# Optimization experiments

Measured on AMD Instinct MI355X. Metric: run time of the kernel, lower is better.

The kernel has to match this reference:

```python
import jax, jax.numpy as jnp
import numpy as np

# (multiplicity, l) segments, ir_mul layout: each segment stored as (2l+1, mul)
IRREPS = [(256, 0), (256, 1), (256, 2), (256, 3)]
BATCH = 8192
DIM = sum(m * (2 * l + 1) for m, l in IRREPS)  # 4096


def _real_basis_U(l):
    """Unitary change of basis from complex to real spherical harmonics (degree l)."""
    n = 2 * l + 1
    U = np.zeros((n, n), dtype=np.complex128)
    U[l, l] = 1.0
    s = 1.0 / np.sqrt(2.0)
    for mu in range(1, l + 1):
        U[l + mu, l - mu] = s
        U[l + mu, l + mu] = s * (-1.0) ** mu
        U[l - mu, l - mu] = 1j * s
        U[l - mu, l + mu] = -1j * s * (-1.0) ** mu
    return U


def _x_generator_eig(l):
    """Eigendecomposition (constants) of the x-axis angular-momentum operator in the real basis."""
    m = np.arange(-l, l + 1)
    n = 2 * l + 1
    Jp = np.zeros((n, n), dtype=np.complex128)
    mm = m[:-1]
    Jp[np.arange(1, n), np.arange(0, n - 1)] = np.sqrt(l * (l + 1) - mm * (mm + 1))
    Jx = (Jp + Jp.conj().T) / 2.0
    U = _real_basis_U(l)
    Jx_r = U @ Jx @ U.conj().T  # Hermitian
    w, V = np.linalg.eigh(Jx_r)  # w = -l..l (integers), V unitary
    return w, V


def _y_rotation(theta, l):
    """Rotation about y in the real irrep basis, built directly from the angle
    encoding [cos(l t),...,cos(t),1,sin(t),...,sin(l t)] -- diag cos(m t), antidiag +/- sin(m t)."""
    B = theta.shape[0]
    n = 2 * l + 1
    mu = jnp.arange(1, l + 1, dtype=theta.dtype)
    c = jnp.cos(mu * theta[:, None])  # [B, l]
    s = jnp.sin(mu * theta[:, None])  # [B, l]
    one = jnp.ones((B, 1), theta.dtype)
    zero = jnp.zeros((B, 1), theta.dtype)
    diag = jnp.concatenate([c[:, ::-1], one, c], axis=-1)    # [B, n]
    anti = jnp.concatenate([-s[:, ::-1], zero, s], axis=-1)  # [B, n]
    idx = jnp.arange(n)
    R = jnp.zeros((B, n, n), theta.dtype)
    R = R.at[:, idx, idx].set(diag)
    R = R.at[:, idx, idx[::-1]].add(anti)
    return R


def _x_rotation(theta, l, dtype):
    """Rotation about x: X(t) = Re(V diag(exp(-i t w)) V^H), done in real arithmetic."""
    w, V = _x_generator_eig(l)
    w = jnp.asarray(w, dtype)
    Vr = jnp.asarray(np.ascontiguousarray(V.real), dtype)
    Vi = jnp.asarray(np.ascontiguousarray(V.imag), dtype)
    C = jnp.cos(theta[:, None] * w)  # [B, n]
    S = jnp.sin(theta[:, None] * w)  # [B, n]
    X = (jnp.einsum('ik,bk,jk->bij', Vr, C, Vr)
         + jnp.einsum('ik,bk,jk->bij', Vi, C, Vi)
         + jnp.einsum('ik,bk,jk->bij', Vi, S, Vr)
         - jnp.einsum('ik,bk,jk->bij', Vr, S, Vi))
    return X


def _rotate(gamma, beta, alpha, x):
    # yxy Euler rotation: first gamma about y, then beta about x, then alpha about y.
    outs = []
    off = 0
    for mul, l in IRREPS:
        n = 2 * l + 1
        seg = x[:, off:off + n * mul].reshape(-1, n, mul)  # ir_mul layout
        D = _y_rotation(alpha, l) @ _x_rotation(beta, l, x.dtype) @ _y_rotation(gamma, l)
        outs.append(jnp.einsum('bij,bjm->bim', D, seg).reshape(-1, n * mul))
        off += n * mul
    return jnp.concatenate(outs, axis=-1)


def setup_inputs() -> dict:
    key = jax.random.key(0)
    kg, kb, ka, kx = jax.random.split(key, 4)
    return {
        'gamma': jax.random.normal(kg, (BATCH,), jnp.float32),
        'beta': jax.random.normal(kb, (BATCH,), jnp.float32),
        'alpha': jax.random.normal(ka, (BATCH,), jnp.float32),
        'x': jax.random.normal(kx, (BATCH, DIM), jnp.float32),
    }


def reference(gamma, beta, alpha, x):
    return _rotate(gamma, beta, alpha, x)
```

## Files before the change

### kernel.cpp

```cpp
#include <hip/hip_runtime.h>
#include <math.h>

#define BATCH 8192
#define DIM 4096


struct FT { float v[495]; };

constexpr double csqrt(double x) {
  double g = x > 1.0 ? x : 1.0;
  for (int i = 0; i < 50; ++i) g = 0.5 * (g + x / g);
  return g;
}

constexpr void mmc(int n, const double* A, const double* B, double* C) {
  for (int i = 0; i < n; ++i)
    for (int j = 0; j < n; ++j) {
      double s = 0.0;
      for (int k = 0; k < n; ++k) s += A[i * n + k] * B[k * n + j];
      C[i * n + j] = s;
    }
}

constexpr FT compute_ft() {
  FT o{};
  for (int l = 1; l <= 3; ++l) {
    const int n = 2 * l + 1, nn = n * n;
    double JX[49] = {}, UR[49] = {}, UI[49] = {};
    for (int a = 0; a < n - 1; ++a) {
      double m = (double)(a - l);
      double v = 0.5 * csqrt((double)(l * (l + 1)) - m * (m + 1.0));
      JX[(a + 1) * n + a] = v;
      JX[a * n + (a + 1)] = v;
    }
    UR[l * n + l] = 1.0;
    const double s = csqrt(0.5);
    for (int mu = 1; mu <= l; ++mu) {
      double sg = (mu & 1) ? -1.0 : 1.0;
      UR[(l + mu) * n + (l - mu)] = s;
      UR[(l + mu) * n + (l + mu)] = s * sg;
      UI[(l - mu) * n + (l - mu)] = s;
      UI[(l - mu) * n + (l + mu)] = -s * sg;
    }
    double MR[49] = {}, MI[49] = {};
    mmc(n, UR, JX, MR);
    mmc(n, UI, JX, MI);
    double K[49] = {};
    for (int a = 0; a < n; ++a)
      for (int b = 0; b < n; ++b) {
        double acc = 0.0;
        for (int c = 0; c < n; ++c)
          acc += MI[a * n + c] * UR[b * n + c] - MR[a * n + c] * UI[b * n + c];
        K[a * n + b] = acc;
      }
    const double TH = 0.78539816339744830962;
    double S[49] = {}, P[49] = {}, T[49] = {};
    for (int i = 0; i < nn; ++i) S[i] = K[i] * (TH / 16.0);
    for (int i = 0; i < n; ++i) P[i * n + i] = 1.0;
    for (int t = 12; t >= 1; --t) {
      mmc(n, S, P, T);
      double inv = 1.0 / (double)t;
      for (int i = 0; i < nn; ++i) P[i] = T[i] * inv;
      for (int i = 0; i < n; ++i) P[i * n + i] += 1.0;
    }
    for (int q = 0; q < 4; ++q) {
      mmc(n, P, P, T);
      for (int i = 0; i < nn; ++i) P[i] = T[i];
    }
    double acc[7][49] = {};
    double Ek[49] = {}, Et[49] = {};
    for (int i = 0; i < n; ++i) Ek[i * n + i] = 1.0;
    const double r2 = csqrt(0.5);
    const double c8[8] = {1.0, r2, 0.0, -r2, -1.0, -r2, 0.0, r2};
    const double s8[8] = {0.0, r2, 1.0, r2, 0.0, -r2, -1.0, -r2};
    for (int k = 0; k < 8; ++k) {
      for (int i = 0; i < nn; ++i) acc[0][i] += 0.125 * Ek[i];
      for (int mu = 1; mu <= l; ++mu) {
        int a8 = (mu * k) & 7;
        double cc = 0.25 * c8[a8], ss = 0.25 * s8[a8];
        for (int i = 0; i < nn; ++i) {
          acc[2 * mu - 1][i] += cc * Ek[i];
          acc[2 * mu][i] += ss * Ek[i];
        }
      }
      mmc(n, Ek, P, Et);
      for (int i = 0; i < nn; ++i) Ek[i] = Et[i];
    }
    int base = (l == 1) ? 0 : ((l == 2) ? 27 : 152);
    for (int t = 0; t <= 2 * l; ++t)
      for (int i = 0; i < nn; ++i) o.v[base + t * nn + i] = (float)acc[t][i];
  }
  return o;
}

__device__ __constant__ FT c_tb = compute_ft();

typedef float vf4 __attribute__((ext_vector_type(4)));

__device__ __forceinline__ vf4 vfma4(float a, vf4 v, vf4 acc) { return acc + a * v; }

__device__ __forceinline__ float entry_for(int e, float cb1, float cb2, float cb3,
                                           float sb1, float sb2, float sb3,
                                           float al, float ga) {
  int l, n, basec, i, j;
  if (e < 9)       { l = 1; n = 3; basec = 0;   int r = e;      i = r / 3; j = r - i * 3; }
  else if (e < 34) { l = 2; n = 5; basec = 27;  int r = e - 9;  i = r / 5; j = r - i * 5; }
  else             { l = 3; n = 7; basec = 152; int r = e - 34; i = r / 7; j = r - i * 7; }

  const float* C = c_tb.v + basec;
  const int ip = n - 1 - i, jp = n - 1 - j;
  const int nn = n * n;
  float xij = 0.f, xijp = 0.f, xipj = 0.f, xipjp = 0.f;
  #pragma unroll
  for (int tt = 0; tt < 7; ++tt) {
    if (tt <= 2 * l) {
      float coef;
      if (tt == 0) coef = 1.f;
      else if (tt == 1) coef = cb1;
      else if (tt == 2) coef = sb1;
      else if (tt == 3) coef = cb2;
      else if (tt == 4) coef = sb2;
      else if (tt == 5) coef = cb3;
      else coef = sb3;
      const float* M = C + tt * nn;
      xij   = fmaf(coef, M[i * n + j],   xij);
      xijp  = fmaf(coef, M[i * n + jp],  xijp);
      xipj  = fmaf(coef, M[ip * n + j],  xipj);
      xipjp = fmaf(coef, M[ip * n + jp], xipjp);
    }
  }
  float sa, ca, sg, cg;
  sincosf((float)(i - l) * al, &sa, &ca);
  sincosf((float)(j - l) * ga, &sg, &cg);
  return (ca * xij + sa * xipj) * cg - (ca * xijp + sa * xipjp) * sg;
}

__device__ __forceinline__ float dget1(float d, int k) {
  return __builtin_bit_cast(
      float, __builtin_amdgcn_readlane(__builtin_bit_cast(int, d), k));
}

__global__ __launch_bounds__(192) void rot_seg(
    const float* __restrict__ gamma, const float* __restrict__ beta,
    const float* __restrict__ alpha, const float* __restrict__ x,
    float* __restrict__ out) {
  const int tid = threadIdx.x;
  const int lane = tid & 63;
  const int wv = tid >> 6;
  const size_t b = (size_t)blockIdx.x;
  const vf4* __restrict__ xin = (const vf4*)x + b * 1024;
  vf4* __restrict__ xo = (vf4*)out + b * 1024;

  const float al = alpha[b], bt = beta[b], ga = gamma[b];

  if (wv == 0) {
    vf4 v0 = xin[lane];
    vf4 v1[3];
    #pragma unroll
    for (int j = 0; j < 3; ++j) v1[j] = xin[64 + j * 64 + lane];
    asm volatile("" ::"v"(v0), "v"(v1[0]), "v"(v1[1]), "v"(v1[2]));

    float cb1, sb1;
    sincosf(bt, &sb1, &cb1);
    int e = lane < 9 ? lane : 8;
    const float d = entry_for(e, cb1, 0.f, 0.f, sb1, 0.f, 0.f, al, ga);

    __builtin_nontemporal_store(v0, &xo[lane]);
    #pragma unroll
    for (int i = 0; i < 3; ++i) {
      vf4 o = (vf4)(0.f);
      #pragma unroll
      for (int j = 0; j < 3; ++j) o = vfma4(dget1(d, i * 3 + j), v1[j], o);
      __builtin_nontemporal_store(o, &xo[64 + i * 64 + lane]);
    }
  } else if (wv == 1) {
    vf4 v2[5];
    #pragma unroll
    for (int j = 0; j < 5; ++j) v2[j] = xin[256 + j * 64 + lane];
    asm volatile("" ::"v"(v2[0]), "v"(v2[1]), "v"(v2[2]), "v"(v2[3]),
                 "v"(v2[4]));

    float cb1, sb1;
    sincosf(bt, &sb1, &cb1);
    const float cb2 = cb1 * cb1 - sb1 * sb1, sb2 = 2.f * sb1 * cb1;
    int e = 9 + (lane < 25 ? lane : 24);
    const float d = entry_for(e, cb1, cb2, 0.f, sb1, sb2, 0.f, al, ga);

    #pragma unroll
    for (int i = 0; i < 5; ++i) {
      vf4 o = (vf4)(0.f);
      #pragma unroll
      for (int j = 0; j < 5; ++j) o = vfma4(dget1(d, i * 5 + j), v2[j], o);
      __builtin_nontemporal_store(o, &xo[256 + i * 64 + lane]);
    }
  } else {
    vf4 v3[7];
    #pragma unroll
    for (int j = 0; j < 7; ++j) v3[j] = xin[576 + j * 64 + lane];
    asm volatile("" ::"v"(v3[0]), "v"(v3[1]), "v"(v3[2]), "v"(v3[3]),
                 "v"(v3[4]), "v"(v3[5]), "v"(v3[6]));

    float cb1, sb1;
    sincosf(bt, &sb1, &cb1);
    const float cb2 = cb1 * cb1 - sb1 * sb1, sb2 = 2.f * sb1 * cb1;
    const float cb3 = cb2 * cb1 - sb2 * sb1, sb3 = sb2 * cb1 + cb2 * sb1;
    int e = 34 + (lane < 49 ? lane : 48);
    const float d = entry_for(e, cb1, cb2, cb3, sb1, sb2, sb3, al, ga);

    #pragma unroll
    for (int i = 0; i < 7; ++i) {
      vf4 o = (vf4)(0.f);
      #pragma unroll
      for (int j = 0; j < 7; ++j) o = vfma4(dget1(d, i * 7 + j), v3[j], o);
      __builtin_nontemporal_store(o, &xo[576 + i * 64 + lane]);
    }
  }
}

extern "C" void kernel_launch(void* const* d_in, const int* in_sizes, int n_in,
                              void* d_out, int out_size, void* d_ws, size_t ws_size,
                              hipStream_t stream) {
  const float* gamma = (const float*)d_in[0];
  const float* beta  = (const float*)d_in[1];
  const float* alpha = (const float*)d_in[2];
  const float* x     = (const float*)d_in[3];
  float* out = (float*)d_out;

  rot_seg<<<BATCH, 192, 0, stream>>>(gamma, beta, alpha, x, out);
}
```

Measured before the change: 43.99 us.

## Process two batch rows per block with load-balanced wave assignment

Each block now handles two batch rows (b and b+BATCH/2) with four waves. Waves 0 and 1 each do the l=0/1 or l=2 segments for both rows, while waves 2 and 3 each do the l=3 segment for one row. This evens out the per-wave work that was lopsided before, where one wave handled 4 vectors and another 7. It also halves the block count. The cost is higher register pressure in waves 0 and 1, which now hold two rows of loaded data.

Result: slower. 74.76 us (+70.0%).

```diff
diff --git a/kernel.cpp b/kernel.cpp
--- a/kernel.cpp
+++ b/kernel.cpp
@@ -140,66 +140,115 @@
       float, __builtin_amdgcn_readlane(__builtin_bit_cast(int, d), k));
 }
 
-__global__ __launch_bounds__(192) void rot_seg(
+__global__ __launch_bounds__(256, 8) void rot_p2(
     const float* __restrict__ gamma, const float* __restrict__ beta,
     const float* __restrict__ alpha, const float* __restrict__ x,
     float* __restrict__ out) {
-  const int tid = threadIdx.x;
-  const int lane = tid & 63;
-  const int wv = tid >> 6;
-  const size_t b = (size_t)blockIdx.x;
-  const vf4* __restrict__ xin = (const vf4*)x + b * 1024;
-  vf4* __restrict__ xo = (vf4*)out + b * 1024;
-
-  const float al = alpha[b], bt = beta[b], ga = gamma[b];
+  const int lane = threadIdx.x & 63;
+  const int wv = threadIdx.x >> 6;
+  const size_t bA = (size_t)blockIdx.x;
+  const size_t bB = bA + BATCH / 2;
+
+  const vf4* __restrict__ xinA = (const vf4*)x + bA * 1024;
+  const vf4* __restrict__ xinB = (const vf4*)x + bB * 1024;
+  vf4* __restrict__ xoA = (vf4*)out + bA * 1024;
+  vf4* __restrict__ xoB = (vf4*)out + bB * 1024;
 
   if (wv == 0) {
-    vf4 v0 = xin[lane];
-    vf4 v1[3];
-    #pragma unroll
-    for (int j = 0; j < 3; ++j) v1[j] = xin[64 + j * 64 + lane];
-    asm volatile("" ::"v"(v0), "v"(v1[0]), "v"(v1[1]), "v"(v1[2]));
-
-    float cb1, sb1;
-    sincosf(bt, &sb1, &cb1);
-    int e = lane < 9 ? lane : 8;
-    const float d = entry_for(e, cb1, 0.f, 0.f, sb1, 0.f, 0.f, al, ga);
-
-    __builtin_nontemporal_store(v0, &xo[lane]);
-    #pragma unroll
-    for (int i = 0; i < 3; ++i) {
-      vf4 o = (vf4)(0.f);
-      #pragma unroll
-      for (int j = 0; j < 3; ++j) o = vfma4(dget1(d, i * 3 + j), v1[j], o);
-      __builtin_nontemporal_store(o, &xo[64 + i * 64 + lane]);
+    vf4 a0 = xinA[lane];
+    vf4 a1[3];
+    #pragma unroll
+    for (int j = 0; j < 3; ++j) a1[j] = xinA[64 + j * 64 + lane];
+    vf4 q0 = xinB[lane];
+    vf4 q1[3];
+    #pragma unroll
+    for (int j = 0; j < 3; ++j) q1[j] = xinB[64 + j * 64 + lane];
+    asm volatile("" ::"v"(a0), "v"(a1[0]), "v"(a1[1]), "v"(a1[2]), "v"(q0),
+                 "v"(q1[0]), "v"(q1[1]), "v"(q1[2]));
+
+    __builtin_nontemporal_store(a0, &xoA[lane]);
+
+    {
+      const float al = alpha[bA], bt = beta[bA], ga = gamma[bA];
+      float cb1, sb1;
+      sincosf(bt, &sb1, &cb1);
+      int e = lane < 9 ? lane : 8;
+      const float d = entry_for(e, cb1, 0.f, 0.f, sb1, 0.f, 0.f, al, ga);
+      #pragma unroll
+      for (int i = 0; i < 3; ++i) {
+        vf4 o = (vf4)(0.f);
+        #pragma unroll
+        for (int j = 0; j < 3; ++j) o = vfma4(dget1(d, i * 3 + j), a1[j], o);
+        __builtin_nontemporal_store(o, &xoA[64 + i * 64 + lane]);
+      }
+    }
+    __builtin_nontemporal_store(q0, &xoB[lane]);
+    {
+      const float al = alpha[bB], bt = beta[bB], ga = gamma[bB];
+      float cb1, sb1;
+      sincosf(bt, &sb1, &cb1);
+      int e = lane < 9 ? lane : 8;
+      const float d = entry_for(e, cb1, 0.f, 0.f, sb1, 0.f, 0.f, al, ga);
+      #pragma unroll
+      for (int i = 0; i < 3; ++i) {
+        vf4 o = (vf4)(0.f);
+        #pragma unroll
+        for (int j = 0; j < 3; ++j) o = vfma4(dget1(d, i * 3 + j), q1[j], o);
+        __builtin_nontemporal_store(o, &xoB[64 + i * 64 + lane]);
+      }
     }
   } else if (wv == 1) {
-    vf4 v2[5];
-    #pragma unroll
-    for (int j = 0; j < 5; ++j) v2[j] = xin[256 + j * 64 + lane];
-    asm volatile("" ::"v"(v2[0]), "v"(v2[1]), "v"(v2[2]), "v"(v2[3]),
-                 "v"(v2[4]));
-
-    float cb1, sb1;
-    sincosf(bt, &sb1, &cb1);
-    const float cb2 = cb1 * cb1 - sb1 * sb1, sb2 = 2.f * sb1 * cb1;
-    int e = 9 + (lane < 25 ? lane : 24);
-    const float d = entry_for(e, cb1, cb2, 0.f, sb1, sb2, 0.f, al, ga);
-
-    #pragma unroll
-    for (int i = 0; i < 5; ++i) {
-      vf4 o = (vf4)(0.f);
-      #pragma unroll
-      for (int j = 0; j < 5; ++j) o = vfma4(dget1(d, i * 5 + j), v2[j], o);
-      __builtin_nontemporal_store(o, &xo[256 + i * 64 + lane]);
+    vf4 a2[5], q2[5];
+    #pragma unroll
+    for (int j = 0; j < 5; ++j) a2[j] = xinA[256 + j * 64 + lane];
+    #pragma unroll
+    for (int j = 0; j < 5; ++j) q2[j] = xinB[256 + j * 64 + lane];
+    asm volatile("" ::"v"(a2[0]), "v"(a2[1]), "v"(a2[2]), "v"(a2[3]),
+                 "v"(a2[4]), "v"(q2[0]), "v"(q2[1]), "v"(q2[2]), "v"(q2[3]),
+                 "v"(q2[4]));
+
+    {
+      const float al = alpha[bA], bt = beta[bA], ga = gamma[bA];
+      float cb1, sb1;
+      sincosf(bt, &sb1, &cb1);
+      const float cb2 = cb1 * cb1 - sb1 * sb1, sb2 = 2.f * sb1 * cb1;
+      int e = 9 + (lane < 25 ? lane : 24);
+      const float d = entry_for(e, cb1, cb2, 0.f, sb1, sb2, 0.f, al, ga);
+      #pragma unroll
+      for (int i = 0; i < 5; ++i) {
+        vf4 o = (vf4)(0.f);
+        #pragma unroll
+        for (int j = 0; j < 5; ++j) o = vfma4(dget1(d, i * 5 + j), a2[j], o);
+        __builtin_nontemporal_store(o, &xoA[256 + i * 64 + lane]);
+      }
+    }
+    {
+      const float al = alpha[bB], bt = beta[bB], ga = gamma[bB];
+      float cb1, sb1;
+      sincosf(bt, &sb1, &cb1);
+      const float cb2 = cb1 * cb1 - sb1 * sb1, sb2 = 2.f * sb1 * cb1;
+      int e = 9 + (lane < 25 ? lane : 24);
+      const float d = entry_for(e, cb1, cb2, 0.f, sb1, sb2, 0.f, al, ga);
+      #pragma unroll
+      for (int i = 0; i < 5; ++i) {
+        vf4 o = (vf4)(0.f);
+        #pragma unroll
+        for (int j = 0; j < 5; ++j) o = vfma4(dget1(d, i * 5 + j), q2[j], o);
+        __builtin_nontemporal_store(o, &xoB[256 + i * 64 + lane]);
+      }
     }
   } else {
+    const size_t b = (wv == 2) ? bA : bB;
+    const vf4* __restrict__ xin = (wv == 2) ? xinA : xinB;
+    vf4* __restrict__ xo = (wv == 2) ? xoA : xoB;
+
     vf4 v3[7];
     #pragma unroll
     for (int j = 0; j < 7; ++j) v3[j] = xin[576 + j * 64 + lane];
     asm volatile("" ::"v"(v3[0]), "v"(v3[1]), "v"(v3[2]), "v"(v3[3]),
                  "v"(v3[4]), "v"(v3[5]), "v"(v3[6]));
 
+    const float al = alpha[b], bt = beta[b], ga = gamma[b];
     float cb1, sb1;
     sincosf(bt, &sb1, &cb1);
     const float cb2 = cb1 * cb1 - sb1 * sb1, sb2 = 2.f * sb1 * cb1;
@@ -226,5 +275,5 @@
   const float* x     = (const float*)d_in[3];
   float* out = (float*)d_out;
 
-  rot_seg<<<BATCH, 192, 0, stream>>>(gamma, beta, alpha, x, out);
-}
+  rot_p2<<<BATCH / 2, 256, 0, stream>>>(gamma, beta, alpha, x, out);
+}
```
